# Kernel optimization log

Hardware: AMD Instinct MI355X
Metric: run time of the kernel (lower is better)

## Reference

```python
import jax, jax.numpy as jnp
import numpy as np

H = 8   # heads
C = 64  # per-head channels (gnn_hidden_dim)
HID = H * C  # 512
IN_CH = 6
EMB = 64
U, M = 16, 512
N_NODES = U * M  # 8192
N_EDGES = 131072


def _tconv(x, src, dst, Wq, bq, Wk, bk, Wv, bv, Ws, bs):
    """PyG TransformerConv (concat=True, root_weight=True, beta=False, eval mode)."""
    N = x.shape[0]
    q = (x @ Wq + bq).reshape(N, H, C)
    k = (x @ Wk + bk).reshape(N, H, C)
    v = (x @ Wv + bv).reshape(N, H, C)
    # per-edge attention scores: query at dst (target i), key at src (source j)
    score = jnp.einsum('ehc,ehc->eh', q[dst], k[src]) / jnp.sqrt(jnp.float32(C))
    # segment softmax over incoming edges of each dst node
    mx = jax.ops.segment_max(score, dst, num_segments=N)
    ex = jnp.exp(score - mx[dst])
    denom = jax.ops.segment_sum(ex, dst, num_segments=N)
    alpha = ex / (denom[dst] + 1e-16)  # [E, H]
    msg = alpha[..., None] * v[src]    # [E, H, C]
    out = jax.ops.segment_sum(msg, dst, num_segments=N).reshape(N, HID)
    return out + x @ Ws + bs  # root/skip connection


def setup_inputs() -> dict:
    key = jax.random.key(0)
    ks = iter(jax.random.split(key, 64))
    s = 0.05

    def lin(k, i, o):
        k1, k2 = jax.random.split(k)
        return (jax.random.normal(k1, (i, o), jnp.float32) * s,
                jax.random.normal(k2, (o,), jnp.float32) * s)

    inp = {}
    inp['mission_coords'] = jax.random.uniform(next(ks), (M, 2), jnp.float32)
    inp['uavs_info'] = jax.random.uniform(next(ks), (U, 2), jnp.float32)
    inp['speeds'] = jax.random.uniform(next(ks), (U,), jnp.float32)
    inp['dist_matrix'] = jax.random.uniform(next(ks), (U, M), jnp.float32)
    inp['timetogo_matrix'] = jax.random.uniform(next(ks), (U, M), jnp.float32)
    inp['action_mask'] = jax.random.randint(next(ks), (U, M), 0, 2, jnp.int32)
    inp['edge_index'] = jax.random.randint(next(ks), (2, N_EDGES), 0, N_NODES, jnp.int64)
    inp['batch'] = jnp.zeros((U,), jnp.int64)

    # layer 0 (in=6)
    inp['Wq0'], inp['bq0'] = lin(next(ks), IN_CH, HID)
    inp['Wk0'], inp['bk0'] = lin(next(ks), IN_CH, HID)
    inp['Wv0'], inp['bv0'] = lin(next(ks), IN_CH, HID)
    inp['Ws0'], inp['bs0'] = lin(next(ks), IN_CH, HID)
    # layers 1..3 stacked (in=512)
    for nm in ['Wq', 'Wk', 'Wv', 'Ws']:
        Ws_, bs_ = [], []
        for _ in range(3):
            w, b = lin(next(ks), HID, HID)
            Ws_.append(w); bs_.append(b)
        inp[nm] = jnp.stack(Ws_)
        inp['b' + nm[1:].lower()] = jnp.stack(bs_)
    inp['Wout'], inp['bout'] = lin(next(ks), HID, EMB)
    inp['Wa1'], inp['ba1'] = lin(next(ks), EMB + 3, 128)
    inp['Wa2'], inp['ba2'] = lin(next(ks), 128, 1)
    inp['Wc1'], inp['bc1'] = lin(next(ks), EMB + 3, 128)
    inp['Wc2'], inp['bc2'] = lin(next(ks), 128, 1)
    return inp


def reference(mission_coords, uavs_info, speeds, dist_matrix, timetogo_matrix,
              action_mask, edge_index, batch,
              Wq0, bq0, Wk0, bk0, Wv0, bv0, Ws0, bs0,
              Wq, bq, Wk, bk, Wv, bv, Ws, bs,
              Wout, bout, Wa1, ba1, Wa2, ba2, Wc1, bc1, Wc2, bc2):
    u, m = uavs_info.shape[0], mission_coords.shape[0]
    mc = jnp.broadcast_to(mission_coords[None], (u, m, 2))
    mask_e = action_mask[..., None].astype(jnp.float32)
    sp_e = jnp.broadcast_to(speeds[:, None, None], (u, m, 1))
    x = jnp.concatenate([mc, mask_e, sp_e, dist_matrix[..., None],
                         timetogo_matrix[..., None]], axis=-1).reshape(u * m, IN_CH)
    src, dst = edge_index[0], edge_index[1]
    x = jax.nn.relu(_tconv(x, src, dst, Wq0, bq0, Wk0, bk0, Wv0, bv0, Ws0, bs0))
    for l in range(3):
        x = jax.nn.relu(_tconv(x, src, dst, Wq[l], bq[l], Wk[l], bk[l],
                               Wv[l], bv[l], Ws[l], bs[l]))
    x = x @ Wout + bout  # [U*M, EMB]
    uav_emb = x.reshape(u, m, EMB).sum(axis=1)  # sum pooling over missions
    combined = jnp.concatenate([uavs_info, uav_emb, speeds[:, None]], axis=-1)
    logits = jax.nn.relu(combined @ Wa1 + ba1) @ Wa2 + ba2  # [U, 1]
    action_probs = jax.nn.softmax(logits, axis=-1)
    state_values = (jax.nn.relu(combined @ Wc1 + bc1) @ Wc2 + bc2).squeeze()
    return action_probs, state_values
```

## Files before the change

### kernel.cpp

```cpp
#include <hip/hip_runtime.h>
#include <hip/hip_bf16.h>
#include <math.h>

#define NNODES 8192
#define NEDGES 131072
#define HID    512
#define UU     16
#define MM     512
#define NQKVS  2048

#if __has_builtin(__builtin_amdgcn_cvt_pk_f32_fp8) && __has_builtin(__builtin_amdgcn_cvt_pk_fp8_f32)
#define HAVE_FP8 1
#else
#define HAVE_FP8 0
#endif

#define KSCALE 16.0f
#define KISCALE (0.125f / 16.0f)

typedef __attribute__((ext_vector_type(8))) short bf16x8;
typedef __attribute__((ext_vector_type(4))) float f32x4;
typedef __attribute__((ext_vector_type(2))) float f32x2;

__device__ __forceinline__ float bf2f(ushort u) {
    return __uint_as_float(((unsigned)u) << 16);
}
__device__ __forceinline__ ushort f2bf(float f) {
    unsigned x = __float_as_uint(f);
    return (ushort)((x + 0x7fffu + ((x >> 16) & 1u)) >> 16);
}

__global__ __launch_bounds__(256) void k_build_x(
    const float* __restrict__ mc, const float* __restrict__ speeds,
    const float* __restrict__ dist, const float* __restrict__ ttg,
    const int* __restrict__ mask, float* __restrict__ x6)
{
    int n = blockIdx.x * blockDim.x + threadIdx.x;
    if (n >= NNODES) return;
    int u = n >> 9, m = n & 511;
    float* o = x6 + (size_t)n * 6;
    o[0] = mc[m * 2 + 0];
    o[1] = mc[m * 2 + 1];
    o[2] = (float)mask[u * MM + m];
    o[3] = speeds[u];
    o[4] = dist[u * MM + m];
    o[5] = ttg[u * MM + m];
}

__global__ __launch_bounds__(256) void k_wt(
    const float* __restrict__ Wq, const float* __restrict__ Wk,
    const float* __restrict__ Wv, const float* __restrict__ Ws,
    ushort* __restrict__ Wt)
{
    __shared__ float tile[64][65];
    int z = blockIdx.z;
    int l = z >> 2, which = z & 3;
    const float* src = (which == 0 ? Wq : which == 1 ? Wk : which == 2 ? Wv : Ws)
                       + (size_t)l * HID * HID;
    int k0 = blockIdx.x * 64, c0 = blockIdx.y * 64;
    int t = threadIdx.x;
#pragma unroll
    for (int i = 0; i < 16; ++i) {
        int idx = i * 256 + t;
        int r = idx >> 6, c = idx & 63;
        tile[r][c] = src[(size_t)(k0 + r) * HID + c0 + c];
    }
    __syncthreads();
    ushort* dst = Wt + ((size_t)l * NQKVS + which * HID + c0) * HID + k0;
#pragma unroll
    for (int i = 0; i < 16; ++i) {
        int idx = i * 256 + t;
        int r = idx >> 6, c = idx & 63;
        dst[(size_t)r * HID + c] = f2bf(tile[c][r]);
    }
}

__global__ __launch_bounds__(256) void k_bias(
    const float* __restrict__ bq, const float* __restrict__ bk,
    const float* __restrict__ bv, const float* __restrict__ bs,
    float* __restrict__ bcat)
{
    int i = blockIdx.x * 256 + threadIdx.x;
    int l = i >> 11, j = i & 2047;
    int which = j >> 9, jj = j & 511;
    const float* b = which == 0 ? bq : which == 1 ? bk : which == 2 ? bv : bs;
    bcat[i] = b[l * HID + jj];
}

__global__ __launch_bounds__(256) void k_lin0(
    const float* __restrict__ x6,
    const float* __restrict__ Wq0, const float* __restrict__ bq0,
    const float* __restrict__ Wk0, const float* __restrict__ bk0,
    const float* __restrict__ Wv0, const float* __restrict__ bv0,
    const float* __restrict__ Ws0, const float* __restrict__ bs0,
    ushort* __restrict__ Y, unsigned char* __restrict__ Kf8)
{
    int n = blockIdx.x;
    int j = threadIdx.x;
    int col0 = j * 8;
    int which = col0 >> 9, jj = col0 & 511;
    const float* W = which == 0 ? Wq0 : which == 1 ? Wk0 : which == 2 ? Wv0 : Ws0;
    const float* b = which == 0 ? bq0 : which == 1 ? bk0 : which == 2 ? bv0 : bs0;
    const float* xr = x6 + (size_t)n * 6;
    float x[6];
#pragma unroll
    for (int t = 0; t < 6; ++t) x[t] = xr[t];
    float s[8];
#pragma unroll
    for (int u = 0; u < 8; ++u) s[u] = b[jj + u];
#pragma unroll
    for (int t = 0; t < 6; ++t)
#pragma unroll
        for (int u = 0; u < 8; ++u)
            s[u] = fmaf(x[t], W[t * HID + jj + u], s[u]);
    bf16x8 o8;
#pragma unroll
    for (int u = 0; u < 8; ++u) o8[u] = (short)f2bf(s[u]);
    *(bf16x8*)(Y + (size_t)n * NQKVS + col0) = o8;
#if HAVE_FP8
    if (which == 1) {
        int w0 = __builtin_amdgcn_cvt_pk_fp8_f32(s[0] * KSCALE, s[1] * KSCALE, 0, false);
        w0     = __builtin_amdgcn_cvt_pk_fp8_f32(s[2] * KSCALE, s[3] * KSCALE, w0, true);
        int w1 = __builtin_amdgcn_cvt_pk_fp8_f32(s[4] * KSCALE, s[5] * KSCALE, 0, false);
        w1     = __builtin_amdgcn_cvt_pk_fp8_f32(s[6] * KSCALE, s[7] * KSCALE, w1, true);
        uint2 uu; uu.x = (unsigned)w0; uu.y = (unsigned)w1;
        *(uint2*)(Kf8 + (size_t)n * HID + jj) = uu;
    }
#endif
}

#define GBM 128
#define GBN 128
#define GBK 64
#define TILEB (GBM * GBK * 2)
#define BUFB  (2 * TILEB)

__device__ __forceinline__ void stage_tile(
    const ushort* __restrict__ Ag, const ushort* __restrict__ Bg,
    char* __restrict__ base, int t)
{
    const int lane = t & 63;
    const int w = t >> 6;
    const int r8 = lane >> 3;
    const int c  = lane & 7;
    const int csw = c ^ r8;
#pragma unroll
    for (int i = 0; i < 4; ++i) {
        int r0 = (w * 4 + i) * 8;
        __builtin_amdgcn_global_load_lds(
            (const __attribute__((address_space(1))) void*)(Ag + (size_t)(r0 + r8) * HID + csw * 8),
            (__attribute__((address_space(3))) void*)(base + r0 * 128 + lane * 16), 16, 0, 0);
        __builtin_amdgcn_global_load_lds(
            (const __attribute__((address_space(1))) void*)(Bg + (size_t)(r0 + r8) * HID + csw * 8),
            (__attribute__((address_space(3))) void*)(base + TILEB + r0 * 128 + lane * 16), 16, 0, 0);
    }
}

__global__ __launch_bounds__(256, 2) void k_gemm(
    const ushort* __restrict__ A,
    const ushort* __restrict__ Bt,
    const float* __restrict__ bias,
    ushort* __restrict__ Y,
    unsigned char* __restrict__ Kf8)
{
    __shared__ char lds[2 * BUFB];
    const int t = threadIdx.x;
    const int bid = blockIdx.x;
    const int xcd = bid & 7;
    const int ii  = bid >> 3;
    const int mi  = (xcd << 3) | (ii & 7);
    const int ni  = ii >> 3;
    const int m0 = mi * GBM, n0 = ni * GBN;

    const int wid = t >> 6, lane = t & 63;
    const int wr = wid >> 1, wc = wid & 1;
    const int l15 = lane & 15, lkq = lane >> 4;

    f32x4 acc[4][4] = {};

    const ushort* Ab = A + (size_t)m0 * HID;
    const ushort* Bb = Bt + (size_t)n0 * HID;

    stage_tile(Ab, Bb, lds, t);
    int cur = 0;
    const int NKS = HID / GBK;
    for (int T = 0; T < NKS; ++T) {
        __syncthreads();
        if (T + 1 < NKS)
            stage_tile(Ab + (T + 1) * GBK, Bb + (T + 1) * GBK,
                       lds + (cur ^ 1) * BUFB, t);
        const char* la = lds + cur * BUFB;
        const char* lb = la + TILEB;
#pragma unroll
        for (int kh = 0; kh < 2; ++kh) {
            const int kq = kh * 4 + lkq;
            const int sw = (kq ^ (l15 & 7)) << 4;
            bf16x8 a[4], b[4];
#pragma unroll
            for (int i = 0; i < 4; ++i)
                a[i] = *(const bf16x8*)(la + (wr * 64 + i * 16 + l15) * 128 + sw);
#pragma unroll
            for (int j = 0; j < 4; ++j)
                b[j] = *(const bf16x8*)(lb + (wc * 64 + j * 16 + l15) * 128 + sw);
#pragma unroll
            for (int i = 0; i < 4; ++i)
#pragma unroll
                for (int j = 0; j < 4; ++j)
                    acc[i][j] = __builtin_amdgcn_mfma_f32_16x16x32_bf16(a[i], b[j], acc[i][j], 0, 0, 0);
        }
        cur ^= 1;
    }

    const bool kquad = ((n0 >> 9) == 1);
#pragma unroll
    for (int i = 0; i < 4; ++i) {
        int row = m0 + wr * 64 + i * 16 + lkq * 4;
#pragma unroll
        for (int j = 0; j < 4; ++j) {
            int col = n0 + wc * 64 + j * 16 + l15;
            float bc = bias[col];
            f32x4 r = acc[i][j];
#pragma unroll
            for (int g = 0; g < 4; ++g) {
                float val = r[g] + bc;
                Y[(size_t)(row + g) * NQKVS + col] = f2bf(val);
#if HAVE_FP8
                if (kquad) {
                    int pk = __builtin_amdgcn_cvt_pk_fp8_f32(val * KSCALE, val * KSCALE, 0, false);
                    Kf8[(size_t)(row + g) * HID + (col - 512)] = (unsigned char)(pk & 0xff);
                }
#endif
            }
        }
    }
}

__global__ __launch_bounds__(256) void k_hist(const int* __restrict__ dst, int* __restrict__ cnt)
{
    int e = blockIdx.x * blockDim.x + threadIdx.x;
    if (e < NEDGES) atomicAdd(&cnt[dst[e]], 1);
}

__global__ __launch_bounds__(256) void k_scan(const int* __restrict__ cnt, int* __restrict__ indptr)
{
    __shared__ int sums[256];
    __shared__ int offs[256];
    int t = threadIdx.x;
    int base = t * 32;
    int s = 0;
    for (int i = 0; i < 32; ++i) s += cnt[base + i];
    sums[t] = s;
    __syncthreads();
    if (t == 0) {
        int run = 0;
        for (int i = 0; i < 256; ++i) { offs[i] = run; run += sums[i]; }
    }
    __syncthreads();
    int off = offs[t];
    for (int i = 0; i < 32; ++i) { indptr[base + i] = off; off += cnt[base + i]; }
    if (t == 255) indptr[NNODES] = off;
}

__global__ __launch_bounds__(256) void k_scatter(
    const int* __restrict__ src, const int* __restrict__ dst,
    const int* __restrict__ indptr, int* __restrict__ cursor, int* __restrict__ ssrc)
{
    int e = blockIdx.x * blockDim.x + threadIdx.x;
    if (e >= NEDGES) return;
    int d = dst[e];
    int p = atomicAdd(&cursor[d], 1);
    ssrc[indptr[d] + p] = src[e];
}

__global__ __launch_bounds__(256) void k_attn(
    const int* __restrict__ indptr, const int* __restrict__ ssrc,
    const ushort* __restrict__ Y,
    const unsigned char* __restrict__ Kf8,
    ushort* __restrict__ X)
{
    int n = blockIdx.x * 4 + (threadIdx.x >> 6);
    if (n >= NNODES) return;
    int l = threadIdx.x & 63;
    int cbase = l * 8;
    const ushort* yq = Y + (size_t)n * NQKVS + cbase;
    float qf[8];
    {
        bf16x8 q8 = *(const bf16x8*)yq;
#pragma unroll
        for (int j = 0; j < 8; ++j) qf[j] = bf2f((ushort)q8[j]);
    }
    float mrun = -INFINITY, ssum = 0.f;
    float acc[8] = {};
    int e0 = indptr[n], e1 = indptr[n + 1];
#if HAVE_FP8
    uint2 ka = {}, kb = {};
#else
    bf16x8 ka = {}, kb = {};
#endif
    bf16x8 va = {}, vb = {};
    if (e0 < e1) {
        int s = ssrc[e0];
#if HAVE_FP8
        ka = *(const uint2*)(Kf8 + (size_t)s * HID + cbase);
#else
        ka = *(const bf16x8*)(Y + (size_t)s * NQKVS + 512 + cbase);
#endif
        va = *(const bf16x8*)(Y + (size_t)s * NQKVS + 1024 + cbase);
    }
    if (e0 + 1 < e1) {
        int s = ssrc[e0 + 1];
#if HAVE_FP8
        kb = *(const uint2*)(Kf8 + (size_t)s * HID + cbase);
#else
        kb = *(const bf16x8*)(Y + (size_t)s * NQKVS + 512 + cbase);
#endif
        vb = *(const bf16x8*)(Y + (size_t)s * NQKVS + 1024 + cbase);
    }
    for (int e = e0; e < e1; ++e) {
        auto k8 = ka; bf16x8 v8 = va;
        ka = kb; va = vb;
        int en = e + 2;
        if (en < e1) {
            int s = ssrc[en];
#if HAVE_FP8
            kb = *(const uint2*)(Kf8 + (size_t)s * HID + cbase);
#else
            kb = *(const bf16x8*)(Y + (size_t)s * NQKVS + 512 + cbase);
#endif
            vb = *(const bf16x8*)(Y + (size_t)s * NQKVS + 1024 + cbase);
        }
        float part = 0.f;
#if HAVE_FP8
        {
            f32x2 k01 = __builtin_amdgcn_cvt_pk_f32_fp8((int)k8.x, false);
            f32x2 k23 = __builtin_amdgcn_cvt_pk_f32_fp8((int)k8.x, true);
            f32x2 k45 = __builtin_amdgcn_cvt_pk_f32_fp8((int)k8.y, false);
            f32x2 k67 = __builtin_amdgcn_cvt_pk_f32_fp8((int)k8.y, true);
            part = fmaf(qf[0], k01.x, part); part = fmaf(qf[1], k01.y, part);
            part = fmaf(qf[2], k23.x, part); part = fmaf(qf[3], k23.y, part);
            part = fmaf(qf[4], k45.x, part); part = fmaf(qf[5], k45.y, part);
            part = fmaf(qf[6], k67.x, part); part = fmaf(qf[7], k67.y, part);
        }
#else
#pragma unroll
        for (int j = 0; j < 8; ++j) part = fmaf(qf[j], bf2f((ushort)k8[j]), part);
#endif
        part += __shfl_xor(part, 1);
        part += __shfl_xor(part, 2);
        part += __shfl_xor(part, 4);
#if HAVE_FP8
        float score = part * KISCALE;
#else
        float score = part * 0.125f;
#endif
        float mnew = fmaxf(mrun, score);
        float sc = __expf(mrun - mnew);
        float p = __expf(score - mnew);
        ssum = ssum * sc + p;
#pragma unroll
        for (int j = 0; j < 8; ++j)
            acc[j] = fmaf(acc[j], sc, p * bf2f((ushort)v8[j]));
        mrun = mnew;
    }
    float inv = ssum > 0.f ? 1.f / ssum : 0.f;
    bf16x8 o8;
#pragma unroll
    for (int j = 0; j < 8; ++j) {
        float o = fmaxf(fmaf(acc[j], inv, bf2f(yq[1536 + j])), 0.f);
        o8[j] = (short)f2bf(o);
    }
    *(bf16x8*)(X + (size_t)n * HID + cbase) = o8;
}

__global__ __launch_bounds__(512) void k_pool(const ushort* __restrict__ X, float* __restrict__ xsumP)
{
    int u = blockIdx.x;
    int pp = blockIdx.y;
    int c = threadIdx.x;
    const ushort* base = X + ((size_t)u * MM + pp * 64) * HID + c;
    float s = 0.f;
    for (int m = 0; m < 64; ++m) s += bf2f(base[(size_t)m * HID]);
    xsumP[((size_t)u * 8 + pp) * HID + c] = s;
}

__global__ __launch_bounds__(512) void k_emb(
    const float* __restrict__ xsumP, const float* __restrict__ Wout,
    const float* __restrict__ bout, float* __restrict__ emb)
{
    __shared__ float xs[HID];
    int u = blockIdx.x, c = threadIdx.x;
    float s = 0.f;
#pragma unroll
    for (int p = 0; p < 8; ++p) s += xsumP[((size_t)u * 8 + p) * HID + c];
    xs[c] = s;
    __syncthreads();
    if (c < 64) {
        float a = 0.f;
        for (int i = 0; i < HID; ++i) a = fmaf(xs[i], Wout[i * 64 + c], a);
        emb[u * 64 + c] = a + 512.0f * bout[c];
    }
}

__global__ __launch_bounds__(128) void k_head(
    const float* __restrict__ uavs, const float* __restrict__ speeds,
    const float* __restrict__ emb,
    const float* __restrict__ Wc1, const float* __restrict__ bc1,
    const float* __restrict__ Wc2, const float* __restrict__ bc2,
    float* __restrict__ out)
{
    __shared__ float comb[67];
    __shared__ float red[128];
    int u = blockIdx.x, t = threadIdx.x;
    if (t < 2) comb[t] = uavs[u * 2 + t];
    else if (t < 66) comb[t] = emb[u * 64 + (t - 2)];
    else if (t == 66) comb[t] = speeds[u];
    __syncthreads();
    float a = bc1[t];
    for (int i = 0; i < 67; ++i) a = fmaf(comb[i], Wc1[i * 128 + t], a);
    a = fmaxf(a, 0.f);
    red[t] = a * Wc2[t];
    __syncthreads();
    for (int sft = 64; sft > 0; sft >>= 1) {
        if (t < sft) red[t] += red[t + sft];
        __syncthreads();
    }
    if (t == 0) {
        out[u]      = 1.0f;
        out[16 + u] = red[0] + bc2[0];
    }
}

extern "C" void kernel_launch(void* const* d_in, const int* in_sizes, int n_in,
                              void* d_out, int out_size, void* d_ws, size_t ws_size,
                              hipStream_t stream)
{
    const float* mission_coords = (const float*)d_in[0];
    const float* uavs_info      = (const float*)d_in[1];
    const float* speeds         = (const float*)d_in[2];
    const float* dist_matrix    = (const float*)d_in[3];
    const float* timetogo       = (const float*)d_in[4];
    const int*   action_mask    = (const int*)d_in[5];
    const int*   edge_index     = (const int*)d_in[6];
    const float* Wq0 = (const float*)d_in[8];  const float* bq0 = (const float*)d_in[9];
    const float* Wk0 = (const float*)d_in[10]; const float* bk0 = (const float*)d_in[11];
    const float* Wv0 = (const float*)d_in[12]; const float* bv0 = (const float*)d_in[13];
    const float* Ws0 = (const float*)d_in[14]; const float* bs0 = (const float*)d_in[15];
    const float* Wq  = (const float*)d_in[16]; const float* bq  = (const float*)d_in[17];
    const float* Wk  = (const float*)d_in[18]; const float* bk  = (const float*)d_in[19];
    const float* Wv  = (const float*)d_in[20]; const float* bv  = (const float*)d_in[21];
    const float* Ws  = (const float*)d_in[22]; const float* bs  = (const float*)d_in[23];
    const float* Wout = (const float*)d_in[24]; const float* bout = (const float*)d_in[25];
    const float* Wc1 = (const float*)d_in[30]; const float* bc1 = (const float*)d_in[31];
    const float* Wc2 = (const float*)d_in[32]; const float* bc2 = (const float*)d_in[33];
    float* out = (float*)d_out;

    const int* e_src = edge_index;
    const int* e_dst = edge_index + NEDGES;

    char* p = (char*)d_ws;
    ushort* Ybf = (ushort*)p;  p += (size_t)NNODES * NQKVS * 2;
    ushort* Xbf = (ushort*)p;  p += (size_t)NNODES * HID * 2;
    ushort* Wt  = (ushort*)p;  p += (size_t)3 * NQKVS * HID * 2;
    unsigned char* Kf8 = (unsigned char*)p; p += (size_t)NNODES * HID;
    float* bcat = (float*)p;   p += (size_t)3 * NQKVS * 4;
    float* x6   = (float*)p;   p += (size_t)NNODES * 6 * 4;
    float* xsumP = (float*)p;  p += (size_t)UU * 8 * HID * 4;
    float* emb  = (float*)p;   p += (size_t)UU * 64 * 4;
    int* cnt    = (int*)p;     p += (size_t)NNODES * 4;
    int* indptr = (int*)p;     p += (size_t)(NNODES + 1) * 4;
    int* cursor = (int*)p;     p += (size_t)NNODES * 4;
    int* ssrc   = (int*)p;     p += (size_t)NEDGES * 4;

    hipMemsetAsync(cnt, 0, NNODES * sizeof(int), stream);
    hipMemsetAsync(cursor, 0, NNODES * sizeof(int), stream);

    k_build_x<<<NNODES / 256, 256, 0, stream>>>(mission_coords, speeds, dist_matrix,
                                                timetogo, action_mask, x6);
    k_wt<<<dim3(8, 8, 12), 256, 0, stream>>>(Wq, Wk, Wv, Ws, Wt);
    k_bias<<<3 * NQKVS / 256, 256, 0, stream>>>(bq, bk, bv, bs, bcat);
    k_hist<<<NEDGES / 256, 256, 0, stream>>>(e_dst, cnt);
    k_scan<<<1, 256, 0, stream>>>(cnt, indptr);
    k_scatter<<<NEDGES / 256, 256, 0, stream>>>(e_src, e_dst, indptr, cursor, ssrc);

    k_lin0<<<NNODES, 256, 0, stream>>>(x6, Wq0, bq0, Wk0, bk0, Wv0, bv0, Ws0, bs0, Ybf, Kf8);
    k_attn<<<NNODES / 4, 256, 0, stream>>>(indptr, ssrc, Ybf, Kf8, Xbf);

    const int ngblocks = (NNODES / GBM) * (NQKVS / GBN);
    for (int l = 0; l < 3; ++l) {
        k_gemm<<<ngblocks, 256, 0, stream>>>(Xbf, Wt + (size_t)l * NQKVS * HID,
                                             bcat + l * NQKVS, Ybf, Kf8);
        k_attn<<<NNODES / 4, 256, 0, stream>>>(indptr, ssrc, Ybf, Kf8, Xbf);
    }

    k_pool<<<dim3(UU, 8), 512, 0, stream>>>(Xbf, xsumP);
    k_emb<<<UU, 512, 0, stream>>>(xsumP, Wout, bout, emb);
    k_head<<<UU, 128, 0, stream>>>(uavs_info, speeds, emb, Wc1, bc1, Wc2, bc2, out);
}
```

Before: 277.3 us.

## Pack K/V into contiguous per-node records and fuse setup and head kernels

K (fp8) and V (bf16) are now written into one interleaved per-node record of 1536 bytes, so the attention gather for each edge reads K and V from a single contiguous row instead of two separate buffers. The setup work is also merged: the bias concat and the zeroing of the count and cursor buffers move into the weight-transpose kernel, which replaces two memsets and a separate kernel. Input construction is folded into k_lin0, and the embedding and head kernels are merged into one. The scan now uses 1024 threads with wavefront shuffles. Together these cut launch count and scattered memory traffic, at the cost of more branching in the GEMM epilogue and scalar byte and short stores to the strided KV layout.

```diff
diff --git a/kernel.cpp b/kernel.cpp
--- a/kernel.cpp
+++ b/kernel.cpp
@@ -8,6 +8,7 @@
 #define UU     16
 #define MM     512
 #define NQKVS  2048
+#define KVREC  1536
 
 #if __has_builtin(__builtin_amdgcn_cvt_pk_f32_fp8) && __has_builtin(__builtin_amdgcn_cvt_pk_fp8_f32)
 #define HAVE_FP8 1
@@ -30,35 +31,34 @@
     return (ushort)((x + 0x7fffu + ((x >> 16) & 1u)) >> 16);
 }
 
-__global__ __launch_bounds__(256) void k_build_x(
-    const float* __restrict__ mc, const float* __restrict__ speeds,
-    const float* __restrict__ dist, const float* __restrict__ ttg,
-    const int* __restrict__ mask, float* __restrict__ x6)
-{
-    int n = blockIdx.x * blockDim.x + threadIdx.x;
-    if (n >= NNODES) return;
-    int u = n >> 9, m = n & 511;
-    float* o = x6 + (size_t)n * 6;
-    o[0] = mc[m * 2 + 0];
-    o[1] = mc[m * 2 + 1];
-    o[2] = (float)mask[u * MM + m];
-    o[3] = speeds[u];
-    o[4] = dist[u * MM + m];
-    o[5] = ttg[u * MM + m];
-}
-
-__global__ __launch_bounds__(256) void k_wt(
+__global__ __launch_bounds__(256) void k_wtb(
     const float* __restrict__ Wq, const float* __restrict__ Wk,
     const float* __restrict__ Wv, const float* __restrict__ Ws,
-    ushort* __restrict__ Wt)
+    const float* __restrict__ bq, const float* __restrict__ bk,
+    const float* __restrict__ bv, const float* __restrict__ bs,
+    ushort* __restrict__ Wt, float* __restrict__ bcat, int* __restrict__ zbuf)
 {
     __shared__ float tile[64][65];
     int z = blockIdx.z;
+    int t = threadIdx.x;
+    if (z == 12) {
+        int id = blockIdx.y * 8 + blockIdx.x;
+        if (id < 24) {
+            int i = id * 256 + t;
+            int l = i >> 11, j = i & 2047;
+            int which = j >> 9, jj = j & 511;
+            const float* b = which == 0 ? bq : which == 1 ? bk : which == 2 ? bv : bs;
+            bcat[i] = b[l * HID + jj];
+        } else if (id < 56) {
+            int idx = (id - 24) * 512 + t * 2;
+            zbuf[idx] = 0; zbuf[idx + 1] = 0;
+        }
+        return;
+    }
     int l = z >> 2, which = z & 3;
     const float* src = (which == 0 ? Wq : which == 1 ? Wk : which == 2 ? Wv : Ws)
                        + (size_t)l * HID * HID;
     int k0 = blockIdx.x * 64, c0 = blockIdx.y * 64;
-    int t = threadIdx.x;
 #pragma unroll
     for (int i = 0; i < 16; ++i) {
         int idx = i * 256 + t;
@@ -75,58 +75,64 @@
     }
 }
 
-__global__ __launch_bounds__(256) void k_bias(
-    const float* __restrict__ bq, const float* __restrict__ bk,
-    const float* __restrict__ bv, const float* __restrict__ bs,
-    float* __restrict__ bcat)
-{
-    int i = blockIdx.x * 256 + threadIdx.x;
-    int l = i >> 11, j = i & 2047;
-    int which = j >> 9, jj = j & 511;
-    const float* b = which == 0 ? bq : which == 1 ? bk : which == 2 ? bv : bs;
-    bcat[i] = b[l * HID + jj];
-}
-
 __global__ __launch_bounds__(256) void k_lin0(
-    const float* __restrict__ x6,
+    const float* __restrict__ mc, const float* __restrict__ speeds,
+    const float* __restrict__ dist, const float* __restrict__ ttg,
+    const int* __restrict__ mask,
     const float* __restrict__ Wq0, const float* __restrict__ bq0,
     const float* __restrict__ Wk0, const float* __restrict__ bk0,
     const float* __restrict__ Wv0, const float* __restrict__ bv0,
     const float* __restrict__ Ws0, const float* __restrict__ bs0,
-    ushort* __restrict__ Y, unsigned char* __restrict__ Kf8)
+    ushort* __restrict__ Y, unsigned char* __restrict__ KV)
 {
     int n = blockIdx.x;
+    int u = n >> 9, m = n & 511;
+    float x[6];
+    x[0] = mc[m * 2 + 0];
+    x[1] = mc[m * 2 + 1];
+    x[2] = (float)mask[u * MM + m];
+    x[3] = speeds[u];
+    x[4] = dist[u * MM + m];
+    x[5] = ttg[u * MM + m];
+
     int j = threadIdx.x;
     int col0 = j * 8;
     int which = col0 >> 9, jj = col0 & 511;
     const float* W = which == 0 ? Wq0 : which == 1 ? Wk0 : which == 2 ? Wv0 : Ws0;
     const float* b = which == 0 ? bq0 : which == 1 ? bk0 : which == 2 ? bv0 : bs0;
-    const float* xr = x6 + (size_t)n * 6;
-    float x[6];
-#pragma unroll
-    for (int t = 0; t < 6; ++t) x[t] = xr[t];
     float s[8];
 #pragma unroll
-    for (int u = 0; u < 8; ++u) s[u] = b[jj + u];
+    for (int uu = 0; uu < 8; ++uu) s[uu] = b[jj + uu];
 #pragma unroll
     for (int t = 0; t < 6; ++t)
 #pragma unroll
-        for (int u = 0; u < 8; ++u)
-            s[u] = fmaf(x[t], W[t * HID + jj + u], s[u]);
-    bf16x8 o8;
-#pragma unroll
-    for (int u = 0; u < 8; ++u) o8[u] = (short)f2bf(s[u]);
-    *(bf16x8*)(Y + (size_t)n * NQKVS + col0) = o8;
+        for (int uu = 0; uu < 8; ++uu)
+            s[uu] = fmaf(x[t], W[t * HID + jj + uu], s[uu]);
+    if (which == 0 || which == 3) {
+        bf16x8 o8;
+#pragma unroll
+        for (int uu = 0; uu < 8; ++uu) o8[uu] = (short)f2bf(s[uu]);
+        *(bf16x8*)(Y + (size_t)n * NQKVS + col0) = o8;
+    } else if (which == 2) {
+        bf16x8 o8;
+#pragma unroll
+        for (int uu = 0; uu < 8; ++uu) o8[uu] = (short)f2bf(s[uu]);
+        *(bf16x8*)(KV + (size_t)n * KVREC + 512 + jj * 2) = o8;
+    } else {
 #if HAVE_FP8
-    if (which == 1) {
         int w0 = __builtin_amdgcn_cvt_pk_fp8_f32(s[0] * KSCALE, s[1] * KSCALE, 0, false);
         w0     = __builtin_amdgcn_cvt_pk_fp8_f32(s[2] * KSCALE, s[3] * KSCALE, w0, true);
         int w1 = __builtin_amdgcn_cvt_pk_fp8_f32(s[4] * KSCALE, s[5] * KSCALE, 0, false);
         w1     = __builtin_amdgcn_cvt_pk_fp8_f32(s[6] * KSCALE, s[7] * KSCALE, w1, true);
-        uint2 uu; uu.x = (unsigned)w0; uu.y = (unsigned)w1;
-        *(uint2*)(Kf8 + (size_t)n * HID + jj) = uu;
-    }
+        uint2 uu2; uu2.x = (unsigned)w0; uu2.y = (unsigned)w1;
+        *(uint2*)(KV + (size_t)n * KVREC + jj) = uu2;
+#else
+        bf16x8 o8;
+#pragma unroll
+        for (int uu = 0; uu < 8; ++uu) o8[uu] = (short)f2bf(s[uu]);
+        *(bf16x8*)(KV + (size_t)n * KVREC + jj * 2) = o8;
 #endif
+    }
 }
 
 #define GBM 128
@@ -161,7 +167,7 @@
     const ushort* __restrict__ Bt,
     const float* __restrict__ bias,
     ushort* __restrict__ Y,
-    unsigned char* __restrict__ Kf8)
+    unsigned char* __restrict__ KV)
 {
     __shared__ char lds[2 * BUFB];
     const int t = threadIdx.x;
@@ -211,7 +217,7 @@
         cur ^= 1;
     }
 
-    const bool kquad = ((n0 >> 9) == 1);
+    const int whichq = n0 >> 9;
 #pragma unroll
     for (int i = 0; i < 4; ++i) {
         int row = m0 + wr * 64 + i * 16 + lkq * 4;
@@ -223,13 +229,18 @@
 #pragma unroll
             for (int g = 0; g < 4; ++g) {
                 float val = r[g] + bc;
-                Y[(size_t)(row + g) * NQKVS + col] = f2bf(val);
+                if (whichq == 0 || whichq == 3) {
+                    Y[(size_t)(row + g) * NQKVS + col] = f2bf(val);
+                } else if (whichq == 2) {
+                    *(ushort*)(KV + (size_t)(row + g) * KVREC + 512 + (col - 1024) * 2) = f2bf(val);
+                } else {
 #if HAVE_FP8
-                if (kquad) {
                     int pk = __builtin_amdgcn_cvt_pk_fp8_f32(val * KSCALE, val * KSCALE, 0, false);
-                    Kf8[(size_t)(row + g) * HID + (col - 512)] = (unsigned char)(pk & 0xff);
+                    KV[(size_t)(row + g) * KVREC + (col - 512)] = (unsigned char)(pk & 0xff);
+#else
+                    *(ushort*)(KV + (size_t)(row + g) * KVREC + (col - 512) * 2) = f2bf(val);
+#endif
                 }
-#endif
             }
         }
     }
@@ -241,24 +252,35 @@
     if (e < NEDGES) atomicAdd(&cnt[dst[e]], 1);
 }
 
-__global__ __launch_bounds__(256) void k_scan(const int* __restrict__ cnt, int* __restrict__ indptr)
-{
-    __shared__ int sums[256];
-    __shared__ int offs[256];
+__global__ __launch_bounds__(1024) void k_scan(const int* __restrict__ cnt, int* __restrict__ indptr)
+{
+    __shared__ int wsum[16];
+    __shared__ int woff[16];
     int t = threadIdx.x;
-    int base = t * 32;
+    int base = t * 8;
+    int v[8];
     int s = 0;
-    for (int i = 0; i < 32; ++i) s += cnt[base + i];
-    sums[t] = s;
+#pragma unroll
+    for (int i = 0; i < 8; ++i) { v[i] = cnt[base + i]; s += v[i]; }
+    int lane = t & 63, w = t >> 6;
+    int incl = s;
+#pragma unroll
+    for (int off = 1; off < 64; off <<= 1) {
+        int u = __shfl_up(incl, off);
+        if (lane >= off) incl += u;
+    }
+    if (lane == 63) wsum[w] = incl;
     __syncthreads();
     if (t == 0) {
         int run = 0;
-        for (int i = 0; i < 256; ++i) { offs[i] = run; run += sums[i]; }
-    }
-    __syncthreads();
-    int off = offs[t];
-    for (int i = 0; i < 32; ++i) { indptr[base + i] = off; off += cnt[base + i]; }
-    if (t == 255) indptr[NNODES] = off;
+#pragma unroll
+        for (int i = 0; i < 16; ++i) { woff[i] = run; run += wsum[i]; }
+    }
+    __syncthreads();
+    int run = woff[w] + incl - s;
+#pragma unroll
+    for (int i = 0; i < 8; ++i) { indptr[base + i] = run; run += v[i]; }
+    if (t == 1023) indptr[NNODES] = run;
 }
 
 __global__ __launch_bounds__(256) void k_scatter(
@@ -275,7 +297,7 @@
 __global__ __launch_bounds__(256) void k_attn(
     const int* __restrict__ indptr, const int* __restrict__ ssrc,
     const ushort* __restrict__ Y,
-    const unsigned char* __restrict__ Kf8,
+    const unsigned char* __restrict__ KV,
     ushort* __restrict__ X)
 {
     int n = blockIdx.x * 4 + (threadIdx.x >> 6);
@@ -294,40 +316,30 @@
     int e0 = indptr[n], e1 = indptr[n + 1];
 #if HAVE_FP8
     uint2 ka = {}, kb = {};
+#define KLOAD(K_, base_) K_ = *(const uint2*)((base_) + cbase)
 #else
     bf16x8 ka = {}, kb = {};
+#define KLOAD(K_, base_) K_ = *(const bf16x8*)((base_) + cbase * 2)
 #endif
     bf16x8 va = {}, vb = {};
     if (e0 < e1) {
-        int s = ssrc[e0];
-#if HAVE_FP8
-        ka = *(const uint2*)(Kf8 + (size_t)s * HID + cbase);
-#else
-        ka = *(const bf16x8*)(Y + (size_t)s * NQKVS + 512 + cbase);
-#endif
-        va = *(const bf16x8*)(Y + (size_t)s * NQKVS + 1024 + cbase);
+        const unsigned char* r = KV + (size_t)ssrc[e0] * KVREC;
+        KLOAD(ka, r);
+        va = *(const bf16x8*)(r + 512 + cbase * 2);
     }
     if (e0 + 1 < e1) {
-        int s = ssrc[e0 + 1];
-#if HAVE_FP8
-        kb = *(const uint2*)(Kf8 + (size_t)s * HID + cbase);
-#else
-        kb = *(const bf16x8*)(Y + (size_t)s * NQKVS + 512 + cbase);
-#endif
-        vb = *(const bf16x8*)(Y + (size_t)s * NQKVS + 1024 + cbase);
+        const unsigned char* r = KV + (size_t)ssrc[e0 + 1] * KVREC;
+        KLOAD(kb, r);
+        vb = *(const bf16x8*)(r + 512 + cbase * 2);
     }
     for (int e = e0; e < e1; ++e) {
         auto k8 = ka; bf16x8 v8 = va;
         ka = kb; va = vb;
         int en = e + 2;
         if (en < e1) {
-            int s = ssrc[en];
-#if HAVE_FP8
-            kb = *(const uint2*)(Kf8 + (size_t)s * HID + cbase);
-#else
-            kb = *(const bf16x8*)(Y + (size_t)s * NQKVS + 512 + cbase);
-#endif
-            vb = *(const bf16x8*)(Y + (size_t)s * NQKVS + 1024 + cbase);
+            const unsigned char* r = KV + (size_t)ssrc[en] * KVREC;
+            KLOAD(kb, r);
+            vb = *(const bf16x8*)(r + 512 + cbase * 2);
         }
         float part = 0.f;
 #if HAVE_FP8
@@ -341,18 +353,16 @@
             part = fmaf(qf[4], k45.x, part); part = fmaf(qf[5], k45.y, part);
             part = fmaf(qf[6], k67.x, part); part = fmaf(qf[7], k67.y, part);
         }
+        const float smul = KISCALE;
 #else
 #pragma unroll
         for (int j = 0; j < 8; ++j) part = fmaf(qf[j], bf2f((ushort)k8[j]), part);
+        const float smul = 0.125f;
 #endif
         part += __shfl_xor(part, 1);
         part += __shfl_xor(part, 2);
         part += __shfl_xor(part, 4);
-#if HAVE_FP8
-        float score = part * KISCALE;
-#else
-        float score = part * 0.125f;
-#endif
+        float score = part * smul;
         float mnew = fmaxf(mrun, score);
         float sc = __expf(mrun - mnew);
         float p = __expf(score - mnew);
@@ -383,11 +393,17 @@
     xsumP[((size_t)u * 8 + pp) * HID + c] = s;
 }
 
-__global__ __launch_bounds__(512) void k_emb(
+__global__ __launch_bounds__(512) void k_embhead(
     const float* __restrict__ xsumP, const float* __restrict__ Wout,
-    const float* __restrict__ bout, float* __restrict__ emb)
+    const float* __restrict__ bout,
+    const float* __restrict__ uavs, const float* __restrict__ speeds,
+    const float* __restrict__ Wc1, const float* __restrict__ bc1,
+    const float* __restrict__ Wc2, const float* __restrict__ bc2,
+    float* __restrict__ out)
 {
     __shared__ float xs[HID];
+    __shared__ float comb[67];
+    __shared__ float red[128];
     int u = blockIdx.x, c = threadIdx.x;
     float s = 0.f;
 #pragma unroll
@@ -397,34 +413,23 @@
     if (c < 64) {
         float a = 0.f;
         for (int i = 0; i < HID; ++i) a = fmaf(xs[i], Wout[i * 64 + c], a);
-        emb[u * 64 + c] = a + 512.0f * bout[c];
-    }
-}
-
-__global__ __launch_bounds__(128) void k_head(
-    const float* __restrict__ uavs, const float* __restrict__ speeds,
-    const float* __restrict__ emb,
-    const float* __restrict__ Wc1, const float* __restrict__ bc1,
-    const float* __restrict__ Wc2, const float* __restrict__ bc2,
-    float* __restrict__ out)
-{
-    __shared__ float comb[67];
-    __shared__ float red[128];
-    int u = blockIdx.x, t = threadIdx.x;
-    if (t < 2) comb[t] = uavs[u * 2 + t];
-    else if (t < 66) comb[t] = emb[u * 64 + (t - 2)];
-    else if (t == 66) comb[t] = speeds[u];
-    __syncthreads();
-    float a = bc1[t];
-    for (int i = 0; i < 67; ++i) a = fmaf(comb[i], Wc1[i * 128 + t], a);
-    a = fmaxf(a, 0.f);
-    red[t] = a * Wc2[t];
+        comb[2 + c] = a + 512.0f * bout[c];
+    }
+    if (c == 64) { comb[0] = uavs[u * 2]; comb[1] = uavs[u * 2 + 1]; }
+    if (c == 65) comb[66] = speeds[u];
+    __syncthreads();
+    if (c < 128) {
+        float a = bc1[c];
+        for (int i = 0; i < 67; ++i) a = fmaf(comb[i], Wc1[i * 128 + c], a);
+        a = fmaxf(a, 0.f);
+        red[c] = a * Wc2[c];
+    }
     __syncthreads();
     for (int sft = 64; sft > 0; sft >>= 1) {
-        if (t < sft) red[t] += red[t + sft];
+        if (c < sft) red[c] += red[c + sft];
         __syncthreads();
     }
-    if (t == 0) {
+    if (c == 0) {
         out[u]      = 1.0f;
         out[16 + u] = red[0] + bc2[0];
     }
@@ -461,38 +466,33 @@
     ushort* Ybf = (ushort*)p;  p += (size_t)NNODES * NQKVS * 2;
     ushort* Xbf = (ushort*)p;  p += (size_t)NNODES * HID * 2;
     ushort* Wt  = (ushort*)p;  p += (size_t)3 * NQKVS * HID * 2;
-    unsigned char* Kf8 = (unsigned char*)p; p += (size_t)NNODES * HID;
+    unsigned char* KV = (unsigned char*)p; p += (size_t)NNODES * KVREC;
     float* bcat = (float*)p;   p += (size_t)3 * NQKVS * 4;
-    float* x6   = (float*)p;   p += (size_t)NNODES * 6 * 4;
     float* xsumP = (float*)p;  p += (size_t)UU * 8 * HID * 4;
-    float* emb  = (float*)p;   p += (size_t)UU * 64 * 4;
     int* cnt    = (int*)p;     p += (size_t)NNODES * 4;
+    int* cursor = (int*)p;     p += (size_t)NNODES * 4;
     int* indptr = (int*)p;     p += (size_t)(NNODES + 1) * 4;
-    int* cursor = (int*)p;     p += (size_t)NNODES * 4;
     int* ssrc   = (int*)p;     p += (size_t)NEDGES * 4;
 
-    hipMemsetAsync(cnt, 0, NNODES * sizeof(int), stream);
-    hipMemsetAsync(cursor, 0, NNODES * sizeof(int), stream);
-
-    k_build_x<<<NNODES / 256, 256, 0, stream>>>(mission_coords, speeds, dist_matrix,
-                                                timetogo, action_mask, x6);
-    k_wt<<<dim3(8, 8, 12), 256, 0, stream>>>(Wq, Wk, Wv, Ws, Wt);
-    k_bias<<<3 * NQKVS / 256, 256, 0, stream>>>(bq, bk, bv, bs, bcat);
+    k_wtb<<<dim3(8, 8, 13), 256, 0, stream>>>(Wq, Wk, Wv, Ws, bq, bk, bv, bs,
+                                              Wt, bcat, cnt);
     k_hist<<<NEDGES / 256, 256, 0, stream>>>(e_dst, cnt);
-    k_scan<<<1, 256, 0, stream>>>(cnt, indptr);
+    k_scan<<<1, 1024, 0, stream>>>(cnt, indptr);
     k_scatter<<<NEDGES / 256, 256, 0, stream>>>(e_src, e_dst, indptr, cursor, ssrc);
 
-    k_lin0<<<NNODES, 256, 0, stream>>>(x6, Wq0, bq0, Wk0, bk0, Wv0, bv0, Ws0, bs0, Ybf, Kf8);
-    k_attn<<<NNODES / 4, 256, 0, stream>>>(indptr, ssrc, Ybf, Kf8, Xbf);
+    k_lin0<<<NNODES, 256, 0, stream>>>(mission_coords, speeds, dist_matrix, timetogo,
+                                       action_mask, Wq0, bq0, Wk0, bk0, Wv0, bv0,
+                                       Ws0, bs0, Ybf, KV);
+    k_attn<<<NNODES / 4, 256, 0, stream>>>(indptr, ssrc, Ybf, KV, Xbf);
 
     const int ngblocks = (NNODES / GBM) * (NQKVS / GBN);
     for (int l = 0; l < 3; ++l) {
         k_gemm<<<ngblocks, 256, 0, stream>>>(Xbf, Wt + (size_t)l * NQKVS * HID,
-                                             bcat + l * NQKVS, Ybf, Kf8);
-        k_attn<<<NNODES / 4, 256, 0, stream>>>(indptr, ssrc, Ybf, Kf8, Xbf);
+                                             bcat + l * NQKVS, Ybf, KV);
+        k_attn<<<NNODES / 4, 256, 0, stream>>>(indptr, ssrc, Ybf, KV, Xbf);
     }
 
     k_pool<<<dim3(UU, 8), 512, 0, stream>>>(Xbf, xsumP);
-    k_emb<<<UU, 512, 0, stream>>>(xsumP, Wout, bout, emb);
-    k_head<<<UU, 128, 0, stream>>>(uavs_info, speeds, emb, Wc1, bc1, Wc2, bc2, out);
-}
+    k_embhead<<<UU, 512, 0, stream>>>(xsumP, Wout, bout, uavs_info, speeds,
+                                      Wc1, bc1, Wc2, bc2, out);
+}
```

New measurement: 268.8 us, median of 2. 3.0% less time.
